# Kernel optimization log

Hardware: AMD Instinct MI355X
Metric: run time of the kernel (lower is better)

## Reference

```python
import jax, jax.numpy as jnp
import numpy as np

N = 50000
E = 800000
G = 2500  # number of graphs


def setup_inputs() -> dict:
    key = jax.random.key(0)
    ks = jax.random.split(key, 10)
    x = jax.random.normal(ks[0], (N, 128), dtype=jnp.float32)
    edge_index = jax.random.randint(ks[1], (2, E), 0, N, dtype=jnp.int64)
    batch = jnp.sort(jax.random.randint(ks[2], (N,), 0, G, dtype=jnp.int64))
    def lin(k, fan_in, shape):
        return jax.random.normal(k, shape, dtype=jnp.float32) / np.sqrt(fan_in)
    return {
        'x': x, 'edge_index': edge_index, 'batch': batch,
        'W1': lin(ks[3], 128, (128, 64)), 'b1': jnp.zeros((64,), jnp.float32),
        'W2': lin(ks[4], 64, (64, 64)),  'b2': jnp.zeros((64,), jnp.float32),
        'W3': lin(ks[5], 64, (64, 64)),  'b3': jnp.zeros((64,), jnp.float32),
        'Wp1': lin(ks[6], 64, (64, 64)), 'bp1': jnp.zeros((64,), jnp.float32),
        'Wp2': lin(ks[7], 64, (64, 32)), 'bp2': jnp.zeros((32,), jnp.float32),
    }


def _gcn_norm(edge_index, n_nodes):
    # PyG GCNConv default: add self-loops, symmetric normalization
    loops = jnp.arange(n_nodes, dtype=edge_index.dtype)
    src = jnp.concatenate([edge_index[0], loops])
    dst = jnp.concatenate([edge_index[1], loops])
    deg = jax.ops.segment_sum(jnp.ones_like(dst, dtype=jnp.float32), dst,
                              num_segments=n_nodes)
    dis = jnp.where(deg > 0, jax.lax.rsqrt(deg), 0.0)
    norm = dis[src] * dis[dst]  # [E + N]
    return src, dst, norm


def _gcn_conv(x, W, b, src, dst, norm, n_nodes):
    h = x @ W                                   # transform first (small dim)
    m = h[src] * norm[:, None]                  # gather + scale
    out = jax.ops.segment_sum(m, dst, num_segments=n_nodes)  # scatter-add
    return out + b


def reference(x, edge_index, batch, W1, b1, W2, b2, W3, b3, Wp1, bp1, Wp2, bp2):
    n_nodes = x.shape[0]
    src, dst, norm = _gcn_norm(edge_index, n_nodes)
    x1 = jax.nn.relu(_gcn_conv(x, W1, b1, src, dst, norm, n_nodes))
    x2 = jax.nn.relu(_gcn_conv(x1, W2, b2, src, dst, norm, n_nodes))
    x3 = jax.nn.relu(_gcn_conv(x2, W3, b3, src, dst, norm, n_nodes))
    h = x1 + x2 + x3
    # global_mean_pool
    sums = jax.ops.segment_sum(h, batch, num_segments=G)
    counts = jax.ops.segment_sum(jnp.ones((n_nodes,), jnp.float32), batch,
                                 num_segments=G)
    pooled = sums / jnp.maximum(counts, 1.0)[:, None]
    z = jax.nn.relu(pooled @ Wp1 + bp1) @ Wp2 + bp2
    return z
```

## Files before the change

### kernel.cpp

```cpp
#include <hip/hip_runtime.h>
#include <math.h>


typedef short short8 __attribute__((ext_vector_type(8)));
typedef float f32x4 __attribute__((ext_vector_type(4)));

__device__ inline float bf2f(unsigned short h) {
    return __uint_as_float((unsigned)h << 16);
}
__device__ inline unsigned short f2bf(float f) {
    unsigned u = __float_as_uint(f);
    return (unsigned short)((u + (0x7FFFu + ((u >> 16) & 1u))) >> 16);
}
__device__ inline unsigned short f2h(float f) {
    union { _Float16 h; unsigned short u; } c;
    c.h = (_Float16)f;
    return c.u;
}
__device__ inline float h2f(unsigned short u) {
    union { unsigned short u; _Float16 h; } c;
    c.u = u;
    return (float)c.h;
}
__device__ inline void bh8f(short8 u, float4& a, float4& b) {
    a.x = bf2f((unsigned short)u[0]); a.y = bf2f((unsigned short)u[1]);
    a.z = bf2f((unsigned short)u[2]); a.w = bf2f((unsigned short)u[3]);
    b.x = bf2f((unsigned short)u[4]); b.y = bf2f((unsigned short)u[5]);
    b.z = bf2f((unsigned short)u[6]); b.w = bf2f((unsigned short)u[7]);
}
__device__ inline float4 f4fma(float s, float4 a, float4 acc) {
    acc.x += s * a.x; acc.y += s * a.y; acc.z += s * a.z; acc.w += s * a.w;
    return acc;
}

__global__ void kA_hist(const int* __restrict__ dst, int* __restrict__ hist,
                        int E, int chunk) {
    __shared__ int h[256];
    int t = threadIdx.x;
    h[t] = 0;
    __syncthreads();
    int e0 = blockIdx.x * chunk;
    int e1 = min(e0 + chunk, E);
    for (int e = e0 + t; e < e1; e += 256) atomicAdd(&h[dst[e] >> 8], 1);
    __syncthreads();
    hist[blockIdx.x * 256 + t] = h[t];
}

__global__ void kA_colscan(const int* __restrict__ hist, int* __restrict__ cursorA,
                           int* __restrict__ tot) {
    __shared__ int s[256];
    int t = threadIdx.x;
    int k = blockIdx.x;
    int v = hist[t * 256 + k];
    s[t] = v;
    __syncthreads();
    for (int st = 1; st < 256; st <<= 1) {
        int u = s[t];
        if (t >= st) u += s[t - st];
        __syncthreads();
        s[t] = u;
        __syncthreads();
    }
    cursorA[t * 256 + k] = s[t] - v;
    if (t == 255) tot[k] = s[255];
}

__global__ void kA_scatter(const int* __restrict__ src, const int* __restrict__ dst,
                           const int* __restrict__ cursorA, const int* __restrict__ tot,
                           unsigned* __restrict__ ebuf, int E, int chunk) {
    __shared__ int s[256];
    __shared__ int cur[256];
    int t = threadIdx.x;
    s[t] = tot[t];
    __syncthreads();
    for (int st = 1; st < 256; st <<= 1) {
        int u = s[t];
        if (t >= st) u += s[t - st];
        __syncthreads();
        s[t] = u;
        __syncthreads();
    }
    int bstart = (t == 0) ? 0 : s[t - 1];
    cur[t] = cursorA[blockIdx.x * 256 + t] + bstart;
    __syncthreads();
    int e0 = blockIdx.x * chunk;
    int e1 = min(e0 + chunk, E);
    for (int e = e0 + t; e < e1; e += 256) {
        int d = dst[e];
        int p = atomicAdd(&cur[d >> 8], 1);
        ebuf[p] = ((unsigned)(d & 255) << 24) | (unsigned)src[e];
    }
}

__global__ void kB1(const unsigned* __restrict__ ebuf, const int* __restrict__ tot,
                    float* __restrict__ dis, int* __restrict__ offs, int N, int E) {
    __shared__ int s[256];
    __shared__ int h[256];
    int t = threadIdx.x;
    int k = blockIdx.x;
    s[t] = tot[t];
    __syncthreads();
    for (int st = 1; st < 256; st <<= 1) {
        int u = s[t];
        if (t >= st) u += s[t - st];
        __syncthreads();
        s[t] = u;
        __syncthreads();
    }
    int lo = (k == 0) ? 0 : s[k - 1];
    int hi = s[k];
    h[t] = 0;
    __syncthreads();
    for (int p = lo + t; p < hi; p += 256) atomicAdd(&h[ebuf[p] >> 24], 1);
    __syncthreads();
    int c = h[t];
    int node = k * 256 + t;
    if (node < N) dis[node] = rsqrtf((float)(c + 1));
    s[t] = c;
    __syncthreads();
    for (int st = 1; st < 256; st <<= 1) {
        int u = s[t];
        if (t >= st) u += s[t - st];
        __syncthreads();
        s[t] = u;
        __syncthreads();
    }
    if (node < N) offs[node] = lo + s[t] - c;
    if (node == N - 1) offs[N] = E;
}

__global__ void kB2(const unsigned* __restrict__ ebuf, const int* __restrict__ tot,
                    const float* __restrict__ dis, const int* __restrict__ offs,
                    unsigned* __restrict__ col, int N, int E) {
    __shared__ int s[256];
    __shared__ int cur[256];
    int t = threadIdx.x;
    int k = blockIdx.x;
    s[t] = tot[t];
    __syncthreads();
    for (int st = 1; st < 256; st <<= 1) {
        int u = s[t];
        if (t >= st) u += s[t - st];
        __syncthreads();
        s[t] = u;
        __syncthreads();
    }
    int lo = (k == 0) ? 0 : s[k - 1];
    int hi = s[k];
    int node = k * 256 + t;
    cur[t] = (node < N) ? offs[node] : 0;
    __syncthreads();
    for (int p = lo + t; p < hi; p += 256) {
        unsigned e = ebuf[p];
        int srcI = (int)(e & 0x00FFFFFFu);
        int q = atomicAdd(&cur[e >> 24], 1);
        col[q] = ((unsigned)f2h(dis[srcI]) << 16) | (unsigned)srcI;
    }
}


template <int K>
__global__ __launch_bounds__(256) void k_gemm_f32(const float* __restrict__ X,
                                                  const float* __restrict__ W,
                                                  unsigned short* __restrict__ H, int n) {
    __shared__ short wt[64 * K];
    int t = threadIdx.x;
    for (int idx = t; idx < 64 * K; idx += 256) {
        int k = idx >> 6, ch = idx & 63;
        wt[ch * K + k] = (short)f2bf(W[idx]);
    }
    __syncthreads();
    int wave = t >> 6, lane = t & 63;
    int q = lane >> 4, l = lane & 15;
    int tile = blockIdx.x * 4 + wave;
    if (tile * 16 >= n) return;
    int node = tile * 16 + l;
    short8 afr[4][K / 32];
#pragma unroll
    for (int mb = 0; mb < 4; mb++)
#pragma unroll
        for (int s = 0; s < K / 32; s++)
            afr[mb][s] = *(const short8*)(wt + (mb * 16 + l) * K + s * 32 + q * 8);
    f32x4 acc[4] = {};
    const float* xr = X + (size_t)node * K + q * 8;
#pragma unroll
    for (int s = 0; s < K / 32; s++) {
        float4 xa = *(const float4*)(xr + s * 32);
        float4 xb = *(const float4*)(xr + s * 32 + 4);
        short8 bfr;
        bfr[0] = (short)f2bf(xa.x); bfr[1] = (short)f2bf(xa.y);
        bfr[2] = (short)f2bf(xa.z); bfr[3] = (short)f2bf(xa.w);
        bfr[4] = (short)f2bf(xb.x); bfr[5] = (short)f2bf(xb.y);
        bfr[6] = (short)f2bf(xb.z); bfr[7] = (short)f2bf(xb.w);
#pragma unroll
        for (int mb = 0; mb < 4; mb++)
            acc[mb] = __builtin_amdgcn_mfma_f32_16x16x32_bf16(afr[mb][s], bfr, acc[mb], 0, 0, 0);
    }
#pragma unroll
    for (int mb = 0; mb < 4; mb++) {
        ushort4 u;
        u.x = f2bf(acc[mb][0]); u.y = f2bf(acc[mb][1]);
        u.z = f2bf(acc[mb][2]); u.w = f2bf(acc[mb][3]);
        ((ushort4*)H)[(size_t)node * 16 + mb * 4 + q] = u;
    }
}

__global__ __launch_bounds__(256) void k_gemm_bf(const unsigned short* __restrict__ Xb,
                                                 const float* __restrict__ W,
                                                 unsigned short* __restrict__ H, int n) {
    const int K = 64;
    __shared__ short wt[64 * K];
    int t = threadIdx.x;
    for (int idx = t; idx < 64 * K; idx += 256) {
        int k = idx >> 6, ch = idx & 63;
        wt[ch * K + k] = (short)f2bf(W[idx]);
    }
    __syncthreads();
    int wave = t >> 6, lane = t & 63;
    int q = lane >> 4, l = lane & 15;
    int tile = blockIdx.x * 4 + wave;
    if (tile * 16 >= n) return;
    int node = tile * 16 + l;
    short8 afr[4][2];
#pragma unroll
    for (int mb = 0; mb < 4; mb++)
#pragma unroll
        for (int s = 0; s < 2; s++)
            afr[mb][s] = *(const short8*)(wt + (mb * 16 + l) * K + s * 32 + q * 8);
    f32x4 acc[4] = {};
    const short8* xr = (const short8*)(Xb + (size_t)node * 64);
#pragma unroll
    for (int s = 0; s < 2; s++) {
        short8 bfr = xr[s * 4 + q];
#pragma unroll
        for (int mb = 0; mb < 4; mb++)
            acc[mb] = __builtin_amdgcn_mfma_f32_16x16x32_bf16(afr[mb][s], bfr, acc[mb], 0, 0, 0);
    }
#pragma unroll
    for (int mb = 0; mb < 4; mb++) {
        ushort4 u;
        u.x = f2bf(acc[mb][0]); u.y = f2bf(acc[mb][1]);
        u.z = f2bf(acc[mb][2]); u.w = f2bf(acc[mb][3]);
        ((ushort4*)H)[(size_t)node * 16 + mb * 4 + q] = u;
    }
}

__global__ void k_agg(const unsigned short* __restrict__ H, const unsigned* __restrict__ col,
                      const int* __restrict__ offs, const float* __restrict__ dis,
                      const float* __restrict__ bias,
                      const unsigned short* __restrict__ add1,
                      const unsigned short* __restrict__ add2,
                      unsigned short* __restrict__ OutB, float* __restrict__ OutS, int n) {
    int t = threadIdx.x;
    int node = blockIdx.x * 32 + (t >> 3);
    if (node >= n) return;
    int lane = t & 7;
    const short8* Hs = (const short8*)H;
    float dn = dis[node];
    float4 acc0, acc1;
    bh8f(Hs[(size_t)node * 8 + lane], acc0, acc1);
    acc0.x *= dn; acc0.y *= dn; acc0.z *= dn; acc0.w *= dn;
    acc1.x *= dn; acc1.y *= dn; acc1.z *= dn; acc1.w *= dn;
    int lo = offs[node], hi = offs[node + 1];
    int p = lo;
    for (; p + 4 <= hi; p += 4) {
        unsigned e0 = col[p], e1 = col[p + 1], e2 = col[p + 2], e3 = col[p + 3];
        short8 g0 = Hs[(size_t)(e0 & 0xFFFFu) * 8 + lane];
        short8 g1 = Hs[(size_t)(e1 & 0xFFFFu) * 8 + lane];
        short8 g2 = Hs[(size_t)(e2 & 0xFFFFu) * 8 + lane];
        short8 g3 = Hs[(size_t)(e3 & 0xFFFFu) * 8 + lane];
        float w0 = h2f((unsigned short)(e0 >> 16));
        float w1 = h2f((unsigned short)(e1 >> 16));
        float w2 = h2f((unsigned short)(e2 >> 16));
        float w3 = h2f((unsigned short)(e3 >> 16));
        float4 a, b;
        bh8f(g0, a, b); acc0 = f4fma(w0, a, acc0); acc1 = f4fma(w0, b, acc1);
        bh8f(g1, a, b); acc0 = f4fma(w1, a, acc0); acc1 = f4fma(w1, b, acc1);
        bh8f(g2, a, b); acc0 = f4fma(w2, a, acc0); acc1 = f4fma(w2, b, acc1);
        bh8f(g3, a, b); acc0 = f4fma(w3, a, acc0); acc1 = f4fma(w3, b, acc1);
    }
    for (; p < hi; p++) {
        unsigned e = col[p];
        float w = h2f((unsigned short)(e >> 16));
        float4 a, b;
        bh8f(Hs[(size_t)(e & 0xFFFFu) * 8 + lane], a, b);
        acc0 = f4fma(w, a, acc0);
        acc1 = f4fma(w, b, acc1);
    }
    const float4* bias4 = (const float4*)bias;
    float4 bb0 = bias4[lane * 2];
    float4 bb1 = bias4[lane * 2 + 1];
    float4 v0, v1;
    v0.x = fmaxf(acc0.x * dn + bb0.x, 0.f);
    v0.y = fmaxf(acc0.y * dn + bb0.y, 0.f);
    v0.z = fmaxf(acc0.z * dn + bb0.z, 0.f);
    v0.w = fmaxf(acc0.w * dn + bb0.w, 0.f);
    v1.x = fmaxf(acc1.x * dn + bb1.x, 0.f);
    v1.y = fmaxf(acc1.y * dn + bb1.y, 0.f);
    v1.z = fmaxf(acc1.z * dn + bb1.z, 0.f);
    v1.w = fmaxf(acc1.w * dn + bb1.w, 0.f);
    size_t slot = (size_t)node * 8 + lane;
    if (OutS) {
        float4 a10, a11, a20, a21;
        bh8f(((const short8*)add1)[slot], a10, a11);
        bh8f(((const short8*)add2)[slot], a20, a21);
        v0.x += a10.x + a20.x; v0.y += a10.y + a20.y;
        v0.z += a10.z + a20.z; v0.w += a10.w + a20.w;
        v1.x += a11.x + a21.x; v1.y += a11.y + a21.y;
        v1.z += a11.z + a21.z; v1.w += a11.w + a21.w;
        float4* S4 = (float4*)OutS;
        size_t oi = (size_t)node * 16 + (size_t)lane * 2;
        S4[oi] = v0;
        S4[oi + 1] = v1;
    } else {
        short8 o;
        o[0] = (short)f2bf(v0.x); o[1] = (short)f2bf(v0.y);
        o[2] = (short)f2bf(v0.z); o[3] = (short)f2bf(v0.w);
        o[4] = (short)f2bf(v1.x); o[5] = (short)f2bf(v1.y);
        o[6] = (short)f2bf(v1.z); o[7] = (short)f2bf(v1.w);
        ((short8*)OutB)[slot] = o;
    }
}

__global__ void k_poolhead(const float* __restrict__ S, const int* __restrict__ batch,
                           const float* __restrict__ Wp1, const float* __restrict__ bp1,
                           const float* __restrict__ Wp2, const float* __restrict__ bp2,
                           float* __restrict__ out, int n, int G) {
    int g = blockIdx.x;
    int j = threadIdx.x;
    int a = 0, b = n;
    while (a < b) { int m = (a + b) >> 1; if (batch[m] < g) a = m + 1; else b = m; }
    int beg = a;
    b = n;
    while (a < b) { int m = (a + b) >> 1; if (batch[m] < g + 1) a = m + 1; else b = m; }
    int end = a;
    float sum = 0.f;
    int i = beg;
    for (; i + 2 <= end; i += 2)
        sum += S[(size_t)i * 64 + j] + S[(size_t)(i + 1) * 64 + j];
    if (i < end) sum += S[(size_t)i * 64 + j];
    float cnt = (float)(end - beg);
    float p = sum / fmaxf(cnt, 1.f);
    __shared__ float ps[64];
    __shared__ float ts[64];
    ps[j] = p;
    __syncthreads();
    float t1 = bp1[j];
#pragma unroll 8
    for (int k = 0; k < 64; k++) t1 += ps[k] * Wp1[k * 64 + j];
    t1 = fmaxf(t1, 0.f);
    ts[j] = t1;
    __syncthreads();
    if (j < 32) {
        float o = bp2[j];
#pragma unroll 8
        for (int k = 0; k < 64; k++) o += ts[k] * Wp2[k * 32 + j];
        out[(size_t)g * 32 + j] = o;
    }
}

extern "C" void kernel_launch(void* const* d_in, const int* in_sizes, int n_in,
                              void* d_out, int out_size, void* d_ws, size_t ws_size,
                              hipStream_t stream) {
    const float* x   = (const float*)d_in[0];
    const int*   ei  = (const int*)d_in[1];
    const int*   bat = (const int*)d_in[2];
    const float* W1  = (const float*)d_in[3];
    const float* b1  = (const float*)d_in[4];
    const float* W2  = (const float*)d_in[5];
    const float* b2  = (const float*)d_in[6];
    const float* W3  = (const float*)d_in[7];
    const float* b3  = (const float*)d_in[8];
    const float* Wp1 = (const float*)d_in[9];
    const float* bp1 = (const float*)d_in[10];
    const float* Wp2 = (const float*)d_in[11];
    const float* bp2 = (const float*)d_in[12];

    int N = in_sizes[0] / 128;
    int E = in_sizes[1] / 2;
    int G = out_size / 32;
    const int* src = ei;
    const int* dst = ei + E;

    char* w = (char*)d_ws;
    auto alloc = [&](size_t bytes) -> void* {
        void* p = (void*)w;
        w += (bytes + 255) & ~(size_t)255;
        return p;
    };
    int NB = (N + 255) / 256;
    int*            offs    = (int*)alloc((size_t)(N + 1) * 4);
    unsigned*       col     = (unsigned*)alloc((size_t)E * 4);
    float*          dis     = (float*)alloc((size_t)N * 4);
    int*            hist    = (int*)alloc((size_t)256 * 256 * 4);
    int*            cursorA = (int*)alloc((size_t)256 * 256 * 4);
    int*            tot     = (int*)alloc((size_t)256 * 4);
    unsigned*       ebuf    = (unsigned*)alloc((size_t)E * 4);
    unsigned short* Hb      = (unsigned short*)alloc((size_t)N * 64 * 2);
    unsigned short* X1      = (unsigned short*)alloc((size_t)N * 64 * 2);
    unsigned short* X2      = (unsigned short*)alloc((size_t)N * 64 * 2);
    float*          S       = (float*)alloc((size_t)N * 64 * 4);

    int chunk = (E + 255) / 256;

    kA_hist<<<256, 256, 0, stream>>>(dst, hist, E, chunk);
    kA_colscan<<<256, 256, 0, stream>>>(hist, cursorA, tot);
    kA_scatter<<<256, 256, 0, stream>>>(src, dst, cursorA, tot, ebuf, E, chunk);
    kB1<<<NB, 256, 0, stream>>>(ebuf, tot, dis, offs, N, E);
    kB2<<<NB, 256, 0, stream>>>(ebuf, tot, dis, offs, col, N, E);

    int ggemm = ((N >> 4) + 3) / 4;
    int gagg  = (N + 31) / 32;
    k_gemm_f32<128><<<ggemm, 256, 0, stream>>>(x, W1, Hb, N);
    k_agg<<<gagg, 256, 0, stream>>>(Hb, col, offs, dis, b1, nullptr, nullptr, X1, nullptr, N);
    k_gemm_bf<<<ggemm, 256, 0, stream>>>(X1, W2, Hb, N);
    k_agg<<<gagg, 256, 0, stream>>>(Hb, col, offs, dis, b2, nullptr, nullptr, X2, nullptr, N);
    k_gemm_bf<<<ggemm, 256, 0, stream>>>(X2, W3, Hb, N);
    k_agg<<<gagg, 256, 0, stream>>>(Hb, col, offs, dis, b3, X1, X2, nullptr, S, N);

    k_poolhead<<<G, 64, 0, stream>>>(S, bat, Wp1, bp1, Wp2, bp2, (float*)d_out, N, G);
}
```

Baseline: 237.0 us.

## Aggregate each node with a full wavefront splitting edges across lanes

The aggregation kernel now gives each node a whole 64-lane wavefront instead of 8 lanes. Eight edge slots each handle 8 feature chunks, every lane processes up to two edges per step, and partial sums are combined with cross-lane shuffle reductions. This targets higher memory-level parallelism on the gather, since average degree is about 16. In exchange it adds shuffle work and leaves 56 of 64 lanes idle during the epilogue. The grid grows eightfold.

```diff
diff --git a/kernel.cpp b/kernel.cpp
--- a/kernel.cpp
+++ b/kernel.cpp
@@ -245,51 +245,66 @@
     }
 }
 
-__global__ void k_agg(const unsigned short* __restrict__ H, const unsigned* __restrict__ col,
-                      const int* __restrict__ offs, const float* __restrict__ dis,
-                      const float* __restrict__ bias,
-                      const unsigned short* __restrict__ add1,
-                      const unsigned short* __restrict__ add2,
-                      unsigned short* __restrict__ OutB, float* __restrict__ OutS, int n) {
-    int t = threadIdx.x;
-    int node = blockIdx.x * 32 + (t >> 3);
+__global__ __launch_bounds__(256) void k_agg(const unsigned short* __restrict__ H,
+                                             const unsigned* __restrict__ col,
+                                             const int* __restrict__ offs,
+                                             const float* __restrict__ dis,
+                                             const float* __restrict__ bias,
+                                             const unsigned short* __restrict__ add1,
+                                             const unsigned short* __restrict__ add2,
+                                             unsigned short* __restrict__ OutB,
+                                             float* __restrict__ OutS, int n) {
+    int t = threadIdx.x;
+    int node = blockIdx.x * 4 + (t >> 6);
     if (node >= n) return;
-    int lane = t & 7;
+    int lane = t & 63;
+    int es = lane >> 3;
+    int cs = lane & 7;
     const short8* Hs = (const short8*)H;
-    float dn = dis[node];
-    float4 acc0, acc1;
-    bh8f(Hs[(size_t)node * 8 + lane], acc0, acc1);
-    acc0.x *= dn; acc0.y *= dn; acc0.z *= dn; acc0.w *= dn;
-    acc1.x *= dn; acc1.y *= dn; acc1.z *= dn; acc1.w *= dn;
+    float4 acc0 = make_float4(0.f, 0.f, 0.f, 0.f);
+    float4 acc1 = make_float4(0.f, 0.f, 0.f, 0.f);
     int lo = offs[node], hi = offs[node + 1];
-    int p = lo;
-    for (; p + 4 <= hi; p += 4) {
-        unsigned e0 = col[p], e1 = col[p + 1], e2 = col[p + 2], e3 = col[p + 3];
-        short8 g0 = Hs[(size_t)(e0 & 0xFFFFu) * 8 + lane];
-        short8 g1 = Hs[(size_t)(e1 & 0xFFFFu) * 8 + lane];
-        short8 g2 = Hs[(size_t)(e2 & 0xFFFFu) * 8 + lane];
-        short8 g3 = Hs[(size_t)(e3 & 0xFFFFu) * 8 + lane];
+    int p = lo + es;
+    for (; p + 8 < hi; p += 16) {
+        unsigned e0 = col[p], e1 = col[p + 8];
+        short8 g0 = Hs[(size_t)(e0 & 0xFFFFu) * 8 + cs];
+        short8 g1 = Hs[(size_t)(e1 & 0xFFFFu) * 8 + cs];
         float w0 = h2f((unsigned short)(e0 >> 16));
         float w1 = h2f((unsigned short)(e1 >> 16));
-        float w2 = h2f((unsigned short)(e2 >> 16));
-        float w3 = h2f((unsigned short)(e3 >> 16));
         float4 a, b;
         bh8f(g0, a, b); acc0 = f4fma(w0, a, acc0); acc1 = f4fma(w0, b, acc1);
         bh8f(g1, a, b); acc0 = f4fma(w1, a, acc0); acc1 = f4fma(w1, b, acc1);
-        bh8f(g2, a, b); acc0 = f4fma(w2, a, acc0); acc1 = f4fma(w2, b, acc1);
-        bh8f(g3, a, b); acc0 = f4fma(w3, a, acc0); acc1 = f4fma(w3, b, acc1);
-    }
-    for (; p < hi; p++) {
+    }
+    if (p < hi) {
         unsigned e = col[p];
         float w = h2f((unsigned short)(e >> 16));
         float4 a, b;
-        bh8f(Hs[(size_t)(e & 0xFFFFu) * 8 + lane], a, b);
+        bh8f(Hs[(size_t)(e & 0xFFFFu) * 8 + cs], a, b);
         acc0 = f4fma(w, a, acc0);
         acc1 = f4fma(w, b, acc1);
     }
+#pragma unroll
+    for (int d = 8; d < 64; d <<= 1) {
+        acc0.x += __shfl_xor(acc0.x, d);
+        acc0.y += __shfl_xor(acc0.y, d);
+        acc0.z += __shfl_xor(acc0.z, d);
+        acc0.w += __shfl_xor(acc0.w, d);
+        acc1.x += __shfl_xor(acc1.x, d);
+        acc1.y += __shfl_xor(acc1.y, d);
+        acc1.z += __shfl_xor(acc1.z, d);
+        acc1.w += __shfl_xor(acc1.w, d);
+    }
+    if (es != 0) return;
+    float dn = dis[node];
+    {
+        float4 a, b;
+        bh8f(Hs[(size_t)node * 8 + cs], a, b);
+        acc0 = f4fma(dn, a, acc0);
+        acc1 = f4fma(dn, b, acc1);
+    }
     const float4* bias4 = (const float4*)bias;
-    float4 bb0 = bias4[lane * 2];
-    float4 bb1 = bias4[lane * 2 + 1];
+    float4 bb0 = bias4[cs * 2];
+    float4 bb1 = bias4[cs * 2 + 1];
     float4 v0, v1;
     v0.x = fmaxf(acc0.x * dn + bb0.x, 0.f);
     v0.y = fmaxf(acc0.y * dn + bb0.y, 0.f);
@@ -299,7 +314,7 @@
     v1.y = fmaxf(acc1.y * dn + bb1.y, 0.f);
     v1.z = fmaxf(acc1.z * dn + bb1.z, 0.f);
     v1.w = fmaxf(acc1.w * dn + bb1.w, 0.f);
-    size_t slot = (size_t)node * 8 + lane;
+    size_t slot = (size_t)node * 8 + cs;
     if (OutS) {
         float4 a10, a11, a20, a21;
         bh8f(((const short8*)add1)[slot], a10, a11);
@@ -309,7 +324,7 @@
         v1.x += a11.x + a21.x; v1.y += a11.y + a21.y;
         v1.z += a11.z + a21.z; v1.w += a11.w + a21.w;
         float4* S4 = (float4*)OutS;
-        size_t oi = (size_t)node * 16 + (size_t)lane * 2;
+        size_t oi = (size_t)node * 16 + (size_t)cs * 2;
         S4[oi] = v0;
         S4[oi + 1] = v1;
     } else {
@@ -410,7 +425,7 @@
     kB2<<<NB, 256, 0, stream>>>(ebuf, tot, dis, offs, col, N, E);
 
     int ggemm = ((N >> 4) + 3) / 4;
-    int gagg  = (N + 31) / 32;
+    int gagg  = (N + 3) / 4;
     k_gemm_f32<128><<<ggemm, 256, 0, stream>>>(x, W1, Hb, N);
     k_agg<<<gagg, 256, 0, stream>>>(Hb, col, offs, dis, b1, nullptr, nullptr, X1, nullptr, N);
     k_gemm_bf<<<ggemm, 256, 0, stream>>>(X1, W2, Hb, N);
```

New measurement: 266.5 us. +12.5%, slower.

## Fuse GCN aggregation with next layer's GEMM via shared-memory staging

Applied to the files above, without the earlier changes.

Merges each aggregation kernel with the following 64x64 bf16 MFMA transform. Each block aggregates 64 nodes, writes the activations both to global memory (for the final residual sum) and to padded LDS, then multiplies them by the next layer's weights. This removes two kernel launches and the global re-read of X1/X2 by the separate GEMM. In exchange it adds a second H buffer and more LDS per block, and each block now processes two node rows serially, which may reduce occupancy for the gather-bound aggregation.

```diff
diff --git a/kernel.cpp b/kernel.cpp
--- a/kernel.cpp
+++ b/kernel.cpp
@@ -157,7 +157,6 @@
         col[q] = ((unsigned)f2h(dis[srcI]) << 16) | (unsigned)srcI;
     }
 }
-
 
 template <int K>
 __global__ __launch_bounds__(256) void k_gemm_f32(const float* __restrict__ X,
@@ -205,33 +204,96 @@
     }
 }
 
-__global__ __launch_bounds__(256) void k_gemm_bf(const unsigned short* __restrict__ Xb,
-                                                 const float* __restrict__ W,
-                                                 unsigned short* __restrict__ H, int n) {
-    const int K = 64;
-    __shared__ short wt[64 * K];
-    int t = threadIdx.x;
-    for (int idx = t; idx < 64 * K; idx += 256) {
+__global__ __launch_bounds__(256) void k_aggemm(const unsigned short* __restrict__ H,
+                                                const unsigned* __restrict__ col,
+                                                const int* __restrict__ offs,
+                                                const float* __restrict__ dis,
+                                                const float* __restrict__ bias,
+                                                const float* __restrict__ W,
+                                                unsigned short* __restrict__ Xout,
+                                                unsigned short* __restrict__ Hout, int n) {
+    __shared__ short wt[64 * 64];
+    __shared__ short vbuf[64 * 72];
+    int t = threadIdx.x;
+    for (int idx = t; idx < 64 * 64; idx += 256) {
         int k = idx >> 6, ch = idx & 63;
-        wt[ch * K + k] = (short)f2bf(W[idx]);
+        wt[ch * 64 + k] = (short)f2bf(W[idx]);
+    }
+    const short8* Hs = (const short8*)H;
+    int base = blockIdx.x * 64;
+    int cs = t & 7;
+    const float4* bias4 = (const float4*)bias;
+    float4 bb0 = bias4[cs * 2];
+    float4 bb1 = bias4[cs * 2 + 1];
+#pragma unroll
+    for (int r = 0; r < 2; r++) {
+        int nl = r * 32 + (t >> 3);
+        int node = base + nl;
+        if (node < n) {
+            float dn = dis[node];
+            float4 acc0, acc1;
+            bh8f(Hs[(size_t)node * 8 + cs], acc0, acc1);
+            acc0.x *= dn; acc0.y *= dn; acc0.z *= dn; acc0.w *= dn;
+            acc1.x *= dn; acc1.y *= dn; acc1.z *= dn; acc1.w *= dn;
+            int lo = offs[node], hi = offs[node + 1];
+            int p = lo;
+            for (; p + 4 <= hi; p += 4) {
+                unsigned e0 = col[p], e1 = col[p + 1], e2 = col[p + 2], e3 = col[p + 3];
+                short8 g0 = Hs[(size_t)(e0 & 0xFFFFu) * 8 + cs];
+                short8 g1 = Hs[(size_t)(e1 & 0xFFFFu) * 8 + cs];
+                short8 g2 = Hs[(size_t)(e2 & 0xFFFFu) * 8 + cs];
+                short8 g3 = Hs[(size_t)(e3 & 0xFFFFu) * 8 + cs];
+                float w0 = h2f((unsigned short)(e0 >> 16));
+                float w1 = h2f((unsigned short)(e1 >> 16));
+                float w2 = h2f((unsigned short)(e2 >> 16));
+                float w3 = h2f((unsigned short)(e3 >> 16));
+                float4 a, b;
+                bh8f(g0, a, b); acc0 = f4fma(w0, a, acc0); acc1 = f4fma(w0, b, acc1);
+                bh8f(g1, a, b); acc0 = f4fma(w1, a, acc0); acc1 = f4fma(w1, b, acc1);
+                bh8f(g2, a, b); acc0 = f4fma(w2, a, acc0); acc1 = f4fma(w2, b, acc1);
+                bh8f(g3, a, b); acc0 = f4fma(w3, a, acc0); acc1 = f4fma(w3, b, acc1);
+            }
+            for (; p < hi; p++) {
+                unsigned e = col[p];
+                float w = h2f((unsigned short)(e >> 16));
+                float4 a, b;
+                bh8f(Hs[(size_t)(e & 0xFFFFu) * 8 + cs], a, b);
+                acc0 = f4fma(w, a, acc0);
+                acc1 = f4fma(w, b, acc1);
+            }
+            float4 v0, v1;
+            v0.x = fmaxf(acc0.x * dn + bb0.x, 0.f);
+            v0.y = fmaxf(acc0.y * dn + bb0.y, 0.f);
+            v0.z = fmaxf(acc0.z * dn + bb0.z, 0.f);
+            v0.w = fmaxf(acc0.w * dn + bb0.w, 0.f);
+            v1.x = fmaxf(acc1.x * dn + bb1.x, 0.f);
+            v1.y = fmaxf(acc1.y * dn + bb1.y, 0.f);
+            v1.z = fmaxf(acc1.z * dn + bb1.z, 0.f);
+            v1.w = fmaxf(acc1.w * dn + bb1.w, 0.f);
+            short8 o;
+            o[0] = (short)f2bf(v0.x); o[1] = (short)f2bf(v0.y);
+            o[2] = (short)f2bf(v0.z); o[3] = (short)f2bf(v0.w);
+            o[4] = (short)f2bf(v1.x); o[5] = (short)f2bf(v1.y);
+            o[6] = (short)f2bf(v1.z); o[7] = (short)f2bf(v1.w);
+            ((short8*)Xout)[(size_t)node * 8 + cs] = o;
+            *(short8*)(vbuf + nl * 72 + cs * 8) = o;
+        }
     }
     __syncthreads();
     int wave = t >> 6, lane = t & 63;
     int q = lane >> 4, l = lane & 15;
-    int tile = blockIdx.x * 4 + wave;
-    if (tile * 16 >= n) return;
-    int node = tile * 16 + l;
+    if (base + wave * 16 >= n) return;
+    int node = base + wave * 16 + l;
     short8 afr[4][2];
 #pragma unroll
     for (int mb = 0; mb < 4; mb++)
 #pragma unroll
         for (int s = 0; s < 2; s++)
-            afr[mb][s] = *(const short8*)(wt + (mb * 16 + l) * K + s * 32 + q * 8);
+            afr[mb][s] = *(const short8*)(wt + (mb * 16 + l) * 64 + s * 32 + q * 8);
     f32x4 acc[4] = {};
-    const short8* xr = (const short8*)(Xb + (size_t)node * 64);
 #pragma unroll
     for (int s = 0; s < 2; s++) {
-        short8 bfr = xr[s * 4 + q];
+        short8 bfr = *(const short8*)(vbuf + (wave * 16 + l) * 72 + s * 32 + q * 8);
 #pragma unroll
         for (int mb = 0; mb < 4; mb++)
             acc[mb] = __builtin_amdgcn_mfma_f32_16x16x32_bf16(afr[mb][s], bfr, acc[mb], 0, 0, 0);
@@ -241,16 +303,16 @@
         ushort4 u;
         u.x = f2bf(acc[mb][0]); u.y = f2bf(acc[mb][1]);
         u.z = f2bf(acc[mb][2]); u.w = f2bf(acc[mb][3]);
-        ((ushort4*)H)[(size_t)node * 16 + mb * 4 + q] = u;
-    }
-}
-
-__global__ void k_agg(const unsigned short* __restrict__ H, const unsigned* __restrict__ col,
-                      const int* __restrict__ offs, const float* __restrict__ dis,
-                      const float* __restrict__ bias,
-                      const unsigned short* __restrict__ add1,
-                      const unsigned short* __restrict__ add2,
-                      unsigned short* __restrict__ OutB, float* __restrict__ OutS, int n) {
+        ((ushort4*)Hout)[(size_t)node * 16 + mb * 4 + q] = u;
+    }
+}
+
+__global__ void k_agg3(const unsigned short* __restrict__ H, const unsigned* __restrict__ col,
+                       const int* __restrict__ offs, const float* __restrict__ dis,
+                       const float* __restrict__ bias,
+                       const unsigned short* __restrict__ add1,
+                       const unsigned short* __restrict__ add2,
+                       float* __restrict__ OutS, int n) {
     int t = threadIdx.x;
     int node = blockIdx.x * 32 + (t >> 3);
     if (node >= n) return;
@@ -300,26 +362,17 @@
     v1.z = fmaxf(acc1.z * dn + bb1.z, 0.f);
     v1.w = fmaxf(acc1.w * dn + bb1.w, 0.f);
     size_t slot = (size_t)node * 8 + lane;
-    if (OutS) {
-        float4 a10, a11, a20, a21;
-        bh8f(((const short8*)add1)[slot], a10, a11);
-        bh8f(((const short8*)add2)[slot], a20, a21);
-        v0.x += a10.x + a20.x; v0.y += a10.y + a20.y;
-        v0.z += a10.z + a20.z; v0.w += a10.w + a20.w;
-        v1.x += a11.x + a21.x; v1.y += a11.y + a21.y;
-        v1.z += a11.z + a21.z; v1.w += a11.w + a21.w;
-        float4* S4 = (float4*)OutS;
-        size_t oi = (size_t)node * 16 + (size_t)lane * 2;
-        S4[oi] = v0;
-        S4[oi + 1] = v1;
-    } else {
-        short8 o;
-        o[0] = (short)f2bf(v0.x); o[1] = (short)f2bf(v0.y);
-        o[2] = (short)f2bf(v0.z); o[3] = (short)f2bf(v0.w);
-        o[4] = (short)f2bf(v1.x); o[5] = (short)f2bf(v1.y);
-        o[6] = (short)f2bf(v1.z); o[7] = (short)f2bf(v1.w);
-        ((short8*)OutB)[slot] = o;
-    }
+    float4 a10, a11, a20, a21;
+    bh8f(((const short8*)add1)[slot], a10, a11);
+    bh8f(((const short8*)add2)[slot], a20, a21);
+    v0.x += a10.x + a20.x; v0.y += a10.y + a20.y;
+    v0.z += a10.z + a20.z; v0.w += a10.w + a20.w;
+    v1.x += a11.x + a21.x; v1.y += a11.y + a21.y;
+    v1.z += a11.z + a21.z; v1.w += a11.w + a21.w;
+    float4* S4 = (float4*)OutS;
+    size_t oi = (size_t)node * 16 + (size_t)lane * 2;
+    S4[oi] = v0;
+    S4[oi + 1] = v1;
 }
 
 __global__ void k_poolhead(const float* __restrict__ S, const int* __restrict__ batch,
@@ -397,6 +450,7 @@
     int*            tot     = (int*)alloc((size_t)256 * 4);
     unsigned*       ebuf    = (unsigned*)alloc((size_t)E * 4);
     unsigned short* Hb      = (unsigned short*)alloc((size_t)N * 64 * 2);
+    unsigned short* Hb2     = (unsigned short*)alloc((size_t)N * 64 * 2);
     unsigned short* X1      = (unsigned short*)alloc((size_t)N * 64 * 2);
     unsigned short* X2      = (unsigned short*)alloc((size_t)N * 64 * 2);
     float*          S       = (float*)alloc((size_t)N * 64 * 4);
@@ -410,13 +464,12 @@
     kB2<<<NB, 256, 0, stream>>>(ebuf, tot, dis, offs, col, N, E);
 
     int ggemm = ((N >> 4) + 3) / 4;
+    int gfuse = (N + 63) / 64;
     int gagg  = (N + 31) / 32;
     k_gemm_f32<128><<<ggemm, 256, 0, stream>>>(x, W1, Hb, N);
-    k_agg<<<gagg, 256, 0, stream>>>(Hb, col, offs, dis, b1, nullptr, nullptr, X1, nullptr, N);
-    k_gemm_bf<<<ggemm, 256, 0, stream>>>(X1, W2, Hb, N);
-    k_agg<<<gagg, 256, 0, stream>>>(Hb, col, offs, dis, b2, nullptr, nullptr, X2, nullptr, N);
-    k_gemm_bf<<<ggemm, 256, 0, stream>>>(X2, W3, Hb, N);
-    k_agg<<<gagg, 256, 0, stream>>>(Hb, col, offs, dis, b3, X1, X2, nullptr, S, N);
+    k_aggemm<<<gfuse, 256, 0, stream>>>(Hb, col, offs, dis, b1, W2, X1, Hb2, N);
+    k_aggemm<<<gfuse, 256, 0, stream>>>(Hb2, col, offs, dis, b2, W3, X2, Hb, N);
+    k_agg3<<<gagg, 256, 0, stream>>>(Hb, col, offs, dis, b3, X1, X2, S, N);
 
     k_poolhead<<<G, 64, 0, stream>>>(S, bat, Wp1, bp1, Wp2, bp2, (float*)d_out, N, G);
 }
```

Result: faster. 227.1 us (-4.2%).
